# Optimization experiments

Hardware: AMD Instinct MI355X
Metric: run time of the kernel (lower is better)

## Reference

```python
import jax, jax.numpy as jnp
import numpy as np

BN_EPS = 1e-5

def setup_inputs() -> dict:
    key = jax.random.key(0)
    ks = jax.random.split(key, 8)
    B, Cin, H, W = 4, 256, 64, 64
    Cqk, Cout = 128, 256
    x = jax.random.normal(ks[0], (B, Cin, H, W), dtype=jnp.float32)
    # 1x1 convs == per-pixel linear maps: weight [out, in], bias [out]
    Wq = jax.random.normal(ks[1], (Cqk, Cin), dtype=jnp.float32) * 0.05
    bq = jax.random.normal(ks[2], (Cqk,), dtype=jnp.float32) * 0.05
    Wk = jax.random.normal(ks[3], (Cqk, Cin), dtype=jnp.float32) * 0.05
    bk = jax.random.normal(ks[4], (Cqk,), dtype=jnp.float32) * 0.05
    Wv = jax.random.normal(ks[5], (Cout, Cin), dtype=jnp.float32) * 0.05
    bv = jax.random.normal(ks[6], (Cout,), dtype=jnp.float32) * 0.05
    gamma = jnp.ones((Cout,), dtype=jnp.float32)
    beta = jnp.zeros((Cout,), dtype=jnp.float32)
    return {"x": x, "Wq": Wq, "bq": bq, "Wk": Wk, "bk": bk,
            "Wv": Wv, "bv": bv, "gamma": gamma, "beta": beta}

def reference(x, Wq, bq, Wk, bk, Wv, bv, gamma, beta):
    B, Cin, H, W = x.shape
    N = H * W
    # 1x1 convs (per-pixel linear projections)
    q = jnp.einsum('bchw,oc->bohw', x, Wq) + bq[None, :, None, None]  # [B,Cqk,H,W]
    k = jnp.einsum('bchw,oc->bohw', x, Wk) + bk[None, :, None, None]  # [B,Cqk,H,W]
    v = jnp.einsum('bchw,oc->bohw', x, Wv) + bv[None, :, None, None]  # [B,Cout,H,W]
    # num_levels=1: bilinear interpolate to the same size is identity.
    qf = q.reshape(B, -1, N)   # [B,Cqk,N]
    kf = k.reshape(B, -1, N)   # [B,Cqk,N]
    vf = v.reshape(B, -1, N)   # [B,Cout,N]
    # score = q^T k, softmax over keys (no 1/sqrt(d) scaling, as in source)
    score = jnp.einsum('bcn,bcm->bnm', qf, kf)        # [B,N,N]
    att = jax.nn.softmax(score, axis=2)               # [B,N,N]
    w = jnp.einsum('bnm,bcm->bcn', att, vf)           # [B,Cout,N]
    merged = w.reshape(B, -1, H, W)                   # [B,Cout,H,W]
    # BatchNorm2d in training mode: batch stats over (B,H,W), biased variance
    mean = jnp.mean(merged, axis=(0, 2, 3), keepdims=True)
    var = jnp.var(merged, axis=(0, 2, 3), keepdims=True)
    norm = (merged - mean) * jax.lax.rsqrt(var + BN_EPS)
    return norm * gamma[None, :, None, None] + beta[None, :, None, None]
```

## Files before the change

kernel.cpp:

```cpp
#include <hip/hip_runtime.h>
#include <hip/hip_bf16.h>

typedef __attribute__((ext_vector_type(8))) _Float16 hfrag;
typedef __attribute__((ext_vector_type(4))) float ffrag;
typedef __attribute__((ext_vector_type(8))) unsigned short us8;
typedef __attribute__((ext_vector_type(4))) unsigned short us4;

#define DEVINL static __device__ __forceinline__
#define MFMAH(a, b, c)  __builtin_amdgcn_mfma_f32_16x16x32_f16((a), (b), (c), 0, 0, 0)

DEVINL void gload_lds16(const _Float16* g, _Float16* l) {
    __builtin_amdgcn_global_load_lds(
        (const __attribute__((address_space(1))) unsigned int*)g,
        (__attribute__((address_space(3))) unsigned int*)l, 16, 0, 0);
}

DEVINL int pkh(float a, float b) {
    typedef __attribute__((ext_vector_type(2))) __fp16 fp16x2;
    fp16x2 t = __builtin_amdgcn_cvt_pkrtz(a, b);
    union { fp16x2 h; int i; } u; u.h = t; return u.i;
}

DEVINL int permV(int p) {
    return (p & 35) | ((p & 8) << 1) | ((p & 4) << 1) | ((p & 16) >> 2);
}

__global__ void kprep(const float* __restrict__ Wq, const float* __restrict__ Wk,
                      const float* __restrict__ Wv, const float* __restrict__ bq,
                      const float* __restrict__ bk, const float* __restrict__ bv,
                      _Float16* __restrict__ Wh, float* __restrict__ ball) {
    int t = blockIdx.x * 256 + threadIdx.x;
    int o = t >> 8, c = t & 255;
    float v = (o < 128) ? Wq[o * 256 + c]
            : (o < 256) ? Wk[(o - 128) * 256 + c]
                        : Wv[(o - 256) * 256 + c];
    Wh[t] = (_Float16)v;
    if (c == 0) {
        ball[o] = (o < 128) ? bq[o] : (o < 256) ? bk[o - 128] : bv[o - 256];
    }
}

__global__ __launch_bounds__(256) void kproj(const float* __restrict__ x,
                                             const _Float16* __restrict__ Wh,
                                             const float* __restrict__ ball,
                                             _Float16* __restrict__ Qb,
                                             _Float16* __restrict__ Kb,
                                             _Float16* __restrict__ Vb) {
    __shared__ _Float16 sX[64 * 256];
    const int t = threadIdx.x;
    const int lane = t & 63;
    const int wv = t >> 6;
    const int l16 = lane & 15;
    const int lg = lane >> 4;
    const int b = blockIdx.x >> 6;
    const int n0 = (blockIdx.x & 63) << 6;
    const float* xb = x + (size_t)b * 256 * 4096 + n0;

    const int p = lane;
#pragma unroll
    for (int ci = 0; ci < 8; ++ci) {
        const int c0 = ci * 32 + (wv << 3);
        __align__(16) _Float16 th[8];
#pragma unroll
        for (int j = 0; j < 8; ++j) th[j] = (_Float16)xb[(size_t)(c0 + j) * 4096 + p];
        *(us8*)&sX[p * 256 + (c0 ^ ((p & 7) << 3))] = *(const us8*)th;
    }
    __syncthreads();

    ffrag accQK[16];
    ffrag accV[16];
#pragma unroll
    for (int i = 0; i < 16; ++i) {
        accQK[i] = ffrag{0.f, 0.f, 0.f, 0.f};
        accV[i]  = ffrag{0.f, 0.f, 0.f, 0.f};
    }
    const int rowx = 16 * wv + l16;
#pragma unroll
    for (int step = 0; step < 8; ++step) {
        const int cb = step * 32 + (lg << 3);
        hfrag ax = *(const hfrag*)&sX[rowx * 256 + (cb ^ ((rowx & 7) << 3))];
#pragma unroll
        for (int ct = 0; ct < 16; ++ct) {
            const int o = ct * 16 + l16;
            hfrag bw = *(const hfrag*)&Wh[o * 256 + cb];
            accQK[ct] = MFMAH(ax, bw, accQK[ct]);
        }
        hfrag bx[4];
#pragma unroll
        for (int c2 = 0; c2 < 4; ++c2) {
            const int px = c2 * 16 + l16;
            bx[c2] = *(const hfrag*)&sX[px * 256 + (cb ^ ((px & 7) << 3))];
        }
#pragma unroll
        for (int mt = 0; mt < 4; ++mt) {
            const int o = 256 + 64 * wv + 16 * mt + l16;
            hfrag aw = *(const hfrag*)&Wh[o * 256 + cb];
#pragma unroll
            for (int c2 = 0; c2 < 4; ++c2)
                accV[mt * 4 + c2] = MFMAH(aw, bx[c2], accV[mt * 4 + c2]);
        }
    }

#pragma unroll
    for (int ct = 0; ct < 16; ++ct) {
        const int o = ct * 16 + l16;
        const float bias = ball[o];
        _Float16* dst = (o < 128) ? Qb : Kb;
        const int oo = o & 127;
#pragma unroll
        for (int r = 0; r < 4; ++r) {
            const int px = 16 * wv + (lg << 2) + r;
            dst[((size_t)b * 4096 + n0 + px) * 128 + oo] = (_Float16)(accQK[ct][r] + bias);
        }
    }
#pragma unroll
    for (int mt = 0; mt < 4; ++mt) {
#pragma unroll
        for (int r = 0; r < 4; ++r) {
            const int o = 64 * wv + 16 * mt + (lg << 2) + r;
            const float bias = ball[256 + o];
#pragma unroll
            for (int c2 = 0; c2 < 4; ++c2) {
                const int px = c2 * 16 + l16;
                Vb[((size_t)b * 256 + o) * 4096 + n0 + permV(px)] =
                    (_Float16)(accV[mt * 4 + c2][r] + bias);
            }
        }
    }
}

__global__ __launch_bounds__(512, 2) void kattn(const _Float16* __restrict__ Qb,
                                                const _Float16* __restrict__ Kb,
                                                const _Float16* __restrict__ Vb,
                                                _Float16* __restrict__ pO,
                                                float* __restrict__ pML) {
    __shared__ __align__(16) _Float16 smem[49664];
    float* sml = (float*)(smem + 49152);

    const int t = threadIdx.x;
    const int lane = t & 63;
    const int wv = t >> 6;
    const int qg = wv & 3;
    const int kh = wv >> 2;
    const int l16 = lane & 15;
    const int lg = lane >> 4;

    const int blk = blockIdx.x;
    const int x8 = blk & 7;
    const int b = x8 >> 1;
    const int ksel = x8 & 1;
    const int qt5 = blk >> 3;
    const int n0 = qt5 << 7;
    const int kb = ksel << 11;

    const _Float16* Kg = Kb + (size_t)b * 4096 * 128;
    const _Float16* Vg = Vb + (size_t)b * 256 * 4096;

    hfrag aq0[4], aq1[4];
    {
        const size_t gq0 = ((size_t)b * 4096 + n0 + qg * 32 + l16) * 128;
        const size_t gq1 = gq0 + 16 * 128;
#pragma unroll
        for (int st = 0; st < 4; ++st) {
            aq0[st] = *(const hfrag*)&Qb[gq0 + st * 32 + lg * 8];
            aq1[st] = *(const hfrag*)&Qb[gq1 + st * 32 + lg * 8];
        }
    }

    float m0 = -3e38f, l0 = 0.f;
    float m1 = -3e38f, l1 = 0.f;
    ffrag O0[16], O1[16];
#pragma unroll
    for (int i = 0; i < 16; ++i) {
        O0[i] = ffrag{0.f, 0.f, 0.f, 0.f};
        O1[i] = ffrag{0.f, 0.f, 0.f, 0.f};
    }

    const int krow_in = lane >> 4;
    const int kcol = lane & 15;
    const int vrow_in = lane >> 3;
    const int vcol = lane & 7;

    auto STAGE = [&](int it, int bsel) {
        const int k0 = kb + (it << 6);
        _Float16* sK = smem + bsel * 24576;
        _Float16* sV = smem + bsel * 24576 + 8192;
#pragma unroll
        for (int j = 0; j < 2; ++j) {
            const int c = 2 * wv + j;
            const int row = 4 * c + krow_in;
            gload_lds16(Kg + (size_t)(k0 + row) * 128 + ((kcol ^ (row & 7)) << 3),
                        sK + c * 512);
        }
#pragma unroll
        for (int j = 0; j < 4; ++j) {
            const int cv = 4 * wv + j;
            const int co = 8 * cv + vrow_in;
            gload_lds16(Vg + (size_t)co * 4096 + k0 + ((vcol ^ (co & 7)) << 3),
                        sV + cv * 512);
        }
    };

    auto COMPUTE = [&](int bsel) {
        const _Float16* sK = smem + bsel * 24576;
        const _Float16* sV = smem + bsel * 24576 + 8192;
        ffrag S00 = ffrag{0.f,0.f,0.f,0.f}, S01 = ffrag{0.f,0.f,0.f,0.f};
        ffrag S10 = ffrag{0.f,0.f,0.f,0.f}, S11 = ffrag{0.f,0.f,0.f,0.f};
#pragma unroll
        for (int kt = 0; kt < 2; ++kt) {
            const int rowk = kh * 32 + kt * 16 + l16;
            const int swz = (rowk & 7) << 3;
#pragma unroll
            for (int st = 0; st < 4; ++st) {
                hfrag ak = *(const hfrag*)&sK[rowk * 128 + ((st * 32 + lg * 8) ^ swz)];
                if (kt == 0) {
                    S00 = MFMAH(ak, aq0[st], S00);
                    S10 = MFMAH(ak, aq1[st], S10);
                } else {
                    S01 = MFMAH(ak, aq0[st], S01);
                    S11 = MFMAH(ak, aq1[st], S11);
                }
            }
        }
        float mx0 = fmaxf(fmaxf(fmaxf(S00[0], S00[1]), fmaxf(S00[2], S00[3])),
                          fmaxf(fmaxf(S01[0], S01[1]), fmaxf(S01[2], S01[3])));
        float mx1 = fmaxf(fmaxf(fmaxf(S10[0], S10[1]), fmaxf(S10[2], S10[3])),
                          fmaxf(fmaxf(S11[0], S11[1]), fmaxf(S11[2], S11[3])));
        mx0 = fmaxf(mx0, __shfl_xor(mx0, 16));
        mx0 = fmaxf(mx0, __shfl_xor(mx0, 32));
        mx1 = fmaxf(mx1, __shfl_xor(mx1, 16));
        mx1 = fmaxf(mx1, __shfl_xor(mx1, 32));
        if (__any((mx0 > m0 + 8.f) || (mx1 > m1 + 8.f))) {
            const float nm0 = fmaxf(m0, mx0), nm1 = fmaxf(m1, mx1);
            const float sc0 = __expf(m0 - nm0), sc1 = __expf(m1 - nm1);
            m0 = nm0; m1 = nm1;
            l0 *= sc0; l1 *= sc1;
#pragma unroll
            for (int i = 0; i < 16; ++i) {
#pragma unroll
                for (int r = 0; r < 4; ++r) {
                    O0[i][r] *= sc0;
                    O1[i][r] *= sc1;
                }
            }
        }
        float e00[4], e01[4], e10[4], e11[4];
        float rs0 = 0.f, rs1 = 0.f;
#pragma unroll
        for (int r = 0; r < 4; ++r) {
            e00[r] = __expf(S00[r] - m0);
            e01[r] = __expf(S01[r] - m0);
            e10[r] = __expf(S10[r] - m1);
            e11[r] = __expf(S11[r] - m1);
            rs0 += e00[r] + e01[r];
            rs1 += e10[r] + e11[r];
        }
        rs0 += __shfl_xor(rs0, 16);
        rs0 += __shfl_xor(rs0, 32);
        rs1 += __shfl_xor(rs1, 16);
        rs1 += __shfl_xor(rs1, 32);
        l0 += rs0;
        l1 += rs1;
        hfrag pb0, pb1;
        {
            union { int i[4]; hfrag h; } u;
            u.i[0] = pkh(e00[0], e00[1]);
            u.i[1] = pkh(e00[2], e00[3]);
            u.i[2] = pkh(e01[0], e01[1]);
            u.i[3] = pkh(e01[2], e01[3]);
            pb0 = u.h;
            u.i[0] = pkh(e10[0], e10[1]);
            u.i[1] = pkh(e10[2], e10[3]);
            u.i[2] = pkh(e11[0], e11[1]);
            u.i[3] = pkh(e11[2], e11[3]);
            pb1 = u.h;
        }
#pragma unroll
        for (int ct = 0; ct < 16; ++ct) {
            const int co = ct * 16 + l16;
            hfrag av = *(const hfrag*)&sV[co * 64 + ((kh * 32 + lg * 8) ^ ((co & 7) << 3))];
            O0[ct] = MFMAH(av, pb0, O0[ct]);
            O1[ct] = MFMAH(av, pb1, O1[ct]);
        }
    };

    STAGE(0, 0);
    __builtin_amdgcn_sched_barrier(0);
#pragma unroll 1
    for (int it = 0; it < 31; ++it) {
        STAGE(it + 1, (it + 1) & 1);
        __builtin_amdgcn_sched_barrier(0);
        asm volatile("s_waitcnt vmcnt(6)" ::: "memory");
        __builtin_amdgcn_s_barrier();
        __builtin_amdgcn_sched_barrier(0);
        COMPUTE(it & 1);
        __builtin_amdgcn_s_barrier();
        __builtin_amdgcn_sched_barrier(0);
    }
    asm volatile("s_waitcnt vmcnt(0)" ::: "memory");
    __builtin_amdgcn_s_barrier();
    COMPUTE(1);

    __syncthreads();
    _Float16* sE = smem;
    const int r0 = qg * 32 + l16;
    const int r1 = r0 + 16;
    const int rsw0 = (r0 & 7) << 3;
    const int rsw1 = (r1 & 7) << 3;
    if (kh == 1) {
        const float inv0 = 1.f / l0, inv1 = 1.f / l1;
#pragma unroll
        for (int ct = 0; ct < 16; ++ct)
#pragma unroll
            for (int r = 0; r < 4; ++r) {
                const int col = ct * 16 + lg * 4 + r;
                sE[r0 * 256 + (col ^ rsw0)] = (_Float16)(O0[ct][r] * inv0);
                sE[r1 * 256 + (col ^ rsw1)] = (_Float16)(O1[ct][r] * inv1);
            }
        if (lg == 0) {
            ((float2*)sml)[r0] = make_float2(m0, l0);
            ((float2*)sml)[r1] = make_float2(m1, l1);
        }
    }
    __syncthreads();
    const size_t mlbase = (size_t)(ksel * 4 + b) * 4096 + n0;
    if (kh == 0) {
        const float2 pml0 = ((const float2*)sml)[r0];
        const float2 pml1 = ((const float2*)sml)[r1];
        const float M0 = fmaxf(m0, pml0.x), M1 = fmaxf(m1, pml1.x);
        const float a0 = __expf(m0 - M0), c0 = __expf(pml0.x - M0);
        const float a1 = __expf(m1 - M1), c1 = __expf(pml1.x - M1);
        const float nl0 = a0 * l0 + c0 * pml0.y;
        const float nl1 = a1 * l1 + c1 * pml1.y;
        const float wa0 = a0 / nl0, wb0 = c0 * pml0.y / nl0;
        const float wa1 = a1 / nl1, wb1 = c1 * pml1.y / nl1;
        if (lg == 0) {
            ((float2*)pML)[mlbase + r0] = make_float2(M0, nl0);
            ((float2*)pML)[mlbase + r1] = make_float2(M1, nl1);
        }
#pragma unroll
        for (int ct = 0; ct < 16; ++ct)
#pragma unroll
            for (int r = 0; r < 4; ++r) {
                const int col = ct * 16 + lg * 4 + r;
                const int i0 = r0 * 256 + (col ^ rsw0);
                const int i1 = r1 * 256 + (col ^ rsw1);
                const float v0 = (float)sE[i0];
                const float v1 = (float)sE[i1];
                sE[i0] = (_Float16)(wa0 * O0[ct][r] + wb0 * v0);
                sE[i1] = (_Float16)(wa1 * O1[ct][r] + wb1 * v1);
            }
    }
    __syncthreads();
    const size_t obase = ((size_t)(ksel * 4 + b) * 4096 + n0) * 256;
#pragma unroll
    for (int i = 0; i < 8; ++i) {
        const int idx = i * 512 + t;
        const int px = idx >> 5;
        const int cg = idx & 31;
        *(us8*)&pO[obase + (size_t)px * 256 + cg * 8] =
            *(const us8*)&sE[px * 256 + (cg ^ (px & 7)) * 8];
    }
}

__global__ __launch_bounds__(256) void kmerge(const _Float16* __restrict__ pO,
                                              const float* __restrict__ pML,
                                              _Float16* __restrict__ wbuf,
                                              float* __restrict__ part) {
    __shared__ float sacc[2048];
    __shared__ float sacc2[2048];
    const int t = threadIdx.x;
    const int rowloc = t >> 5;
    const int co8 = (t & 31) * 8;
    float s[8], s2[8];
#pragma unroll
    for (int j = 0; j < 8; ++j) { s[j] = 0.f; s2[j] = 0.f; }
#pragma unroll 2
    for (int i = 0; i < 8; ++i) {
        const int g = blockIdx.x * 64 + i * 8 + rowloc;
        const float2 ml0 = ((const float2*)pML)[g];
        const float2 ml1 = ((const float2*)pML)[16384 + g];
        const float M = fmaxf(ml0.x, ml1.x);
        const float a = __expf(ml0.x - M) * ml0.y;
        const float c = __expf(ml1.x - M) * ml1.y;
        const float inv = 1.f / (a + c);
        const float wa = a * inv, wc = c * inv;
        hfrag o0 = *(const hfrag*)&pO[(size_t)g * 256 + co8];
        hfrag o1 = *(const hfrag*)&pO[(size_t)(16384 + g) * 256 + co8];
        hfrag w;
#pragma unroll
        for (int j = 0; j < 8; ++j) {
            const float v = wa * (float)o0[j] + wc * (float)o1[j];
            w[j] = (_Float16)v;
            s[j] += v;
            s2[j] += v * v;
        }
        *(hfrag*)&wbuf[(size_t)g * 256 + co8] = w;
    }
#pragma unroll
    for (int j = 0; j < 8; ++j) {
        sacc[rowloc * 256 + co8 + j] = s[j];
        sacc2[rowloc * 256 + co8 + j] = s2[j];
    }
    __syncthreads();
    float p = 0.f, p2 = 0.f;
#pragma unroll
    for (int rl = 0; rl < 8; ++rl) {
        p  += sacc[rl * 256 + t];
        p2 += sacc2[rl * 256 + t];
    }
    part[blockIdx.x * 512 + t] = p;
    part[blockIdx.x * 512 + 256 + t] = p2;
}

__global__ void kstats2(const float* __restrict__ partial, float* __restrict__ stats) {
    const int ch = blockIdx.x;
    const int j = threadIdx.x;
    float s = 0.f;
#pragma unroll
    for (int i = 0; i < 4; ++i)
        s += partial[(size_t)(j + 64 * i) * 512 + ch];
    s += __shfl_xor(s, 1);
    s += __shfl_xor(s, 2);
    s += __shfl_xor(s, 4);
    s += __shfl_xor(s, 8);
    s += __shfl_xor(s, 16);
    s += __shfl_xor(s, 32);
    if (j == 0) stats[ch] = s;
}

__global__ __launch_bounds__(256) void kapply(const _Float16* __restrict__ w,
                                              const float* __restrict__ stats,
                                              const float* __restrict__ gamma,
                                              const float* __restrict__ beta,
                                              float* __restrict__ out) {
    __shared__ _Float16 sw[64 * 260];
    __shared__ float sscale[256];
    __shared__ float sshift[256];
    const int t = threadIdx.x;
    const int b = blockIdx.x >> 6;
    const int n0 = (blockIdx.x & 63) << 6;
    const _Float16* wb = w + ((size_t)b * 4096 + n0) * 256;
#pragma unroll
    for (int i = 0; i < 16; ++i) {
        const int chunk = i * 256 + t;
        const int p = chunk >> 6;
        const int cq = chunk & 63;
        *(us4*)&sw[p * 260 + cq * 4] = *(const us4*)&wb[p * 256 + cq * 4];
    }
    {
        const float mean = stats[t] * (1.f / 16384.f);
        const float var = stats[256 + t] * (1.f / 16384.f) - mean * mean;
        const float inv = rsqrtf(var + 1e-5f);
        const float sc = gamma[t] * inv;
        sscale[t] = sc;
        sshift[t] = beta[t] - mean * sc;
    }
    __syncthreads();
    const int p = t & 63;
    const int cg = t >> 6;
    float* ob = out + (size_t)b * 256 * 4096 + n0;
#pragma unroll 4
    for (int i = 0; i < 64; ++i) {
        const int co = i * 4 + cg;
        const float v = (float)sw[p * 260 + co];
        ob[(size_t)co * 4096 + p] = v * sscale[co] + sshift[co];
    }
}

extern "C" void kernel_launch(void* const* d_in, const int* in_sizes, int n_in,
                              void* d_out, int out_size, void* d_ws, size_t ws_size,
                              hipStream_t stream) {
    const float* x     = (const float*)d_in[0];
    const float* Wq    = (const float*)d_in[1];
    const float* bq    = (const float*)d_in[2];
    const float* Wk    = (const float*)d_in[3];
    const float* bk    = (const float*)d_in[4];
    const float* Wv    = (const float*)d_in[5];
    const float* bv    = (const float*)d_in[6];
    const float* gamma = (const float*)d_in[7];
    const float* beta  = (const float*)d_in[8];
    float* out = (float*)d_out;

    char* ws = (char*)d_ws;
    _Float16* Wh    = (_Float16*)(ws + 0x0);
    float*    pML   = (float*)(ws + 0x0);
    float*    ball  = (float*)(ws + 0x40000);
    float*    stats = (float*)(ws + 0x40800);
    float*    part  = (float*)(ws + 0x41000);
    _Float16* Qb    = (_Float16*)(ws + 0x100000);
    _Float16* Kb    = (_Float16*)(ws + 0x500000);
    _Float16* wbuf  = (_Float16*)(ws + 0x100000);
    _Float16* Vb    = (_Float16*)(ws + 0x900000);
    _Float16* pO    = (_Float16*)(ws + 0x1100000);
    if (ws_size < 0x2100000) return;

    kprep<<<512, 256, 0, stream>>>(Wq, Wk, Wv, bq, bk, bv, Wh, ball);
    kproj<<<256, 256, 0, stream>>>(x, Wh, ball, Qb, Kb, Vb);
    kattn<<<256, 512, 0, stream>>>(Qb, Kb, Vb, pO, pML);
    kmerge<<<256, 256, 0, stream>>>(pO, pML, wbuf, part);
    kstats2<<<512, 64, 0, stream>>>(part, stats);
    kapply<<<256, 256, 0, stream>>>(wbuf, stats, gamma, beta, out);
}
```

Before: 138.2 us.

## Software-pipeline flash attention: overlap QK of next tile with PV of previous

```diff
diff --git a/kernel.cpp b/kernel.cpp
--- a/kernel.cpp
+++ b/kernel.cpp
@@ -175,16 +175,16 @@
         O0[i] = ffrag{0.f, 0.f, 0.f, 0.f};
         O1[i] = ffrag{0.f, 0.f, 0.f, 0.f};
     }
+    hfrag pb0p, pb1p;
 
     const int krow_in = lane >> 4;
     const int kcol = lane & 15;
     const int vrow_in = lane >> 3;
     const int vcol = lane & 7;
 
-    auto STAGE = [&](int it, int bsel) {
+    auto STAGEK = [&](int it, int bsel) {
         const int k0 = kb + (it << 6);
-        _Float16* sK = smem + bsel * 24576;
-        _Float16* sV = smem + bsel * 24576 + 8192;
+        _Float16* sK = smem + (bsel << 13);
 #pragma unroll
         for (int j = 0; j < 2; ++j) {
             const int c = 2 * wv + j;
@@ -192,6 +192,10 @@
             gload_lds16(Kg + (size_t)(k0 + row) * 128 + ((kcol ^ (row & 7)) << 3),
                         sK + c * 512);
         }
+    };
+    auto STAGEV = [&](int it, int bsel) {
+        const int k0 = kb + (it << 6);
+        _Float16* sV = smem + 16384 + (bsel << 14);
 #pragma unroll
         for (int j = 0; j < 4; ++j) {
             const int cv = 4 * wv + j;
@@ -201,9 +205,32 @@
         }
     };
 
-    auto COMPUTE = [&](int bsel) {
-        const _Float16* sK = smem + bsel * 24576;
-        const _Float16* sV = smem + bsel * 24576 + 8192;
+    auto PV = [&](int bsel) {
+        const _Float16* sV = smem + 16384 + (bsel << 14);
+#pragma unroll
+        for (int ct = 0; ct < 16; ++ct) {
+            const int co = ct * 16 + l16;
+            hfrag av = *(const hfrag*)&sV[co * 64 + ((kh * 32 + lg * 8) ^ ((co & 7) << 3))];
+            O0[ct] = MFMAH(av, pb0p, O0[ct]);
+            O1[ct] = MFMAH(av, pb1p, O1[ct]);
+        }
+    };
+
+    STAGEK(0, 0);
+    STAGEV(0, 0);
+    __builtin_amdgcn_sched_barrier(0);
+
+#pragma unroll 1
+    for (int it = 0; it < 32; ++it) {
+        asm volatile("s_waitcnt vmcnt(4)" ::: "memory");
+        __builtin_amdgcn_s_barrier();
+        __builtin_amdgcn_sched_barrier(0);
+        STAGEK((it + 1) & 31, (it + 1) & 1);
+        __builtin_amdgcn_sched_barrier(0);
+
+        const _Float16* sK = smem + ((it & 1) << 13);
+
+        __builtin_amdgcn_s_setprio(1);
         ffrag S00 = ffrag{0.f,0.f,0.f,0.f}, S01 = ffrag{0.f,0.f,0.f,0.f};
         ffrag S10 = ffrag{0.f,0.f,0.f,0.f}, S11 = ffrag{0.f,0.f,0.f,0.f};
 #pragma unroll
@@ -222,6 +249,9 @@
                 }
             }
         }
+        if (it > 0) PV((it - 1) & 1);
+        __builtin_amdgcn_s_setprio(0);
+
         float mx0 = fmaxf(fmaxf(fmaxf(S00[0], S00[1]), fmaxf(S00[2], S00[3])),
                           fmaxf(fmaxf(S01[0], S01[1]), fmaxf(S01[2], S01[3])));
         float mx1 = fmaxf(fmaxf(fmaxf(S10[0], S10[1]), fmaxf(S10[2], S10[3])),
@@ -261,45 +291,30 @@
         rs1 += __shfl_xor(rs1, 32);
         l0 += rs0;
         l1 += rs1;
-        hfrag pb0, pb1;
+
         {
             union { int i[4]; hfrag h; } u;
             u.i[0] = pkh(e00[0], e00[1]);
             u.i[1] = pkh(e00[2], e00[3]);
             u.i[2] = pkh(e01[0], e01[1]);
             u.i[3] = pkh(e01[2], e01[3]);
-            pb0 = u.h;
+            pb0p = u.h;
             u.i[0] = pkh(e10[0], e10[1]);
             u.i[1] = pkh(e10[2], e10[3]);
             u.i[2] = pkh(e11[0], e11[1]);
             u.i[3] = pkh(e11[2], e11[3]);
-            pb1 = u.h;
-        }
-#pragma unroll
-        for (int ct = 0; ct < 16; ++ct) {
-            const int co = ct * 16 + l16;
-            hfrag av = *(const hfrag*)&sV[co * 64 + ((kh * 32 + lg * 8) ^ ((co & 7) << 3))];
-            O0[ct] = MFMAH(av, pb0, O0[ct]);
-            O1[ct] = MFMAH(av, pb1, O1[ct]);
-        }
-    };
-
-    STAGE(0, 0);
-    __builtin_amdgcn_sched_barrier(0);
-#pragma unroll 1
-    for (int it = 0; it < 31; ++it) {
-        STAGE(it + 1, (it + 1) & 1);
-        __builtin_amdgcn_sched_barrier(0);
-        asm volatile("s_waitcnt vmcnt(6)" ::: "memory");
+            pb1p = u.h;
+        }
+
         __builtin_amdgcn_s_barrier();
         __builtin_amdgcn_sched_barrier(0);
-        COMPUTE(it & 1);
-        __builtin_amdgcn_s_barrier();
+        STAGEV((it + 1) & 31, (it + 1) & 1);
         __builtin_amdgcn_sched_barrier(0);
     }
+
     asm volatile("s_waitcnt vmcnt(0)" ::: "memory");
     __builtin_amdgcn_s_barrier();
-    COMPUTE(1);
+    PV(1);
 
     __syncthreads();
     _Float16* sE = smem;
```

Result: faster. 134.8 us (median of 3 runs) (-2.4%).
